# Kernel tuning notes

Measured on AMD Instinct MI355X. Metric: run time of the kernel, lower is better.

The kernel has to match this reference:

```python
import jax, jax.numpy as jnp
import numpy as np

NUM_HEADS = 16
D_MODEL = 1024
SEQ = 4096
HEAD_DIM = D_MODEL // NUM_HEADS
ROPE_BASE = 10000.0


def _rope(x):
    # x: [h, s, d]  (rotate-half RoPE per head)
    s, d = x.shape[-2], x.shape[-1]
    inv_freq = 1.0 / (ROPE_BASE ** (jnp.arange(0, d, 2, dtype=jnp.float32) / d))  # [d/2]
    ang = jnp.arange(s, dtype=jnp.float32)[:, None] * inv_freq[None, :]           # [s, d/2]
    cos, sin = jnp.cos(ang), jnp.sin(ang)
    x1, x2 = x[..., : d // 2], x[..., d // 2 :]
    return jnp.concatenate([x1 * cos - x2 * sin, x1 * sin + x2 * cos], axis=-1)


def setup_inputs() -> dict:
    key = jax.random.key(0)
    kq, kk, kv, kwq, kwk, kwv = jax.random.split(key, 6)
    scale = 1.0 / np.sqrt(D_MODEL)
    return {
        "q": jax.random.normal(kq, (SEQ, D_MODEL), dtype=jnp.float32),
        "k": jax.random.normal(kk, (SEQ, D_MODEL), dtype=jnp.float32),
        "v": jax.random.normal(kv, (SEQ, D_MODEL), dtype=jnp.float32),
        "mask": jnp.tril(jnp.ones((SEQ, SEQ), dtype=bool)),  # causal
        "Wq": jax.random.normal(kwq, (D_MODEL, D_MODEL), dtype=jnp.float32) * scale,
        "Wk": jax.random.normal(kwk, (D_MODEL, D_MODEL), dtype=jnp.float32) * scale,
        "Wv": jax.random.normal(kwv, (D_MODEL, D_MODEL), dtype=jnp.float32) * scale,
    }


def reference(q, k, v, mask, Wq, Wk, Wv):
    # Projections (eqx Linear: x @ W.T, no bias)
    qp = q @ Wq.T  # [s, d_model]
    kp = k @ Wk.T
    vp = v @ Wv.T
    # split heads: [s, (h d)] -> [h, s, d]
    def split(x):
        return x.reshape(SEQ, NUM_HEADS, HEAD_DIM).transpose(1, 0, 2)
    qh, kh, vh = split(qp), split(kp), split(vp)
    qh = _rope(qh)
    kh = _rope(kh)
    # explicit full logits, masked softmax (matches original, no SDPA)
    logits = jnp.einsum("hqd,hkd->hqk", qh, kh) / jnp.sqrt(jnp.float32(HEAD_DIM))
    logits = jnp.where(mask[None, :, :], logits, -jnp.inf)
    attn = jax.nn.softmax(logits, axis=-1)  # [h, q, k]
    out = jnp.einsum("hqk,hkd->hqd", attn, vh)
    return out.transpose(1, 0, 2).reshape(SEQ, D_MODEL)
```

## Files before the change

### kernel.cpp

```cpp
#include <hip/hip_runtime.h>
#include <math.h>

#define SEQ 4096
#define DMODEL 1024
#define NHEADS 16
#define HDIM 64

typedef __bf16 v8bf __attribute__((ext_vector_type(8)));
typedef float f32x4 __attribute__((ext_vector_type(4)));
typedef float f32x16 __attribute__((ext_vector_type(16)));
typedef int i32x2 __attribute__((ext_vector_type(2)));
typedef int i32x4 __attribute__((ext_vector_type(4)));

#define NPART 4608
#define SCALE_Q 0.18033688011112042f

__device__ __forceinline__ unsigned short f2bf(float f) {
    union { float f; unsigned int u; } v; v.f = f;
    unsigned int u = v.u;
    return (unsigned short)((u + 0x7fffu + ((u >> 16) & 1u)) >> 16);
}

__device__ __forceinline__ int cvtpk(float lo, float hi) {
    int r;
    asm("v_cvt_pk_bf16_f32 %0, %1, %2" : "=v"(r) : "v"(lo), "v"(hi));
    return r;
}

__device__ __forceinline__ void gload16(const unsigned short* g, unsigned short* l) {
    __builtin_amdgcn_global_load_lds(
        (const __attribute__((address_space(1))) unsigned int*)g,
        (__attribute__((address_space(3))) unsigned int*)l, 16, 0, 0);
}

__global__ __launch_bounds__(256) void cast_kernel(
    const float* __restrict__ q, const float* __restrict__ k, const float* __restrict__ v,
    const float* __restrict__ wq, const float* __restrict__ wk, const float* __restrict__ wv,
    unsigned short* __restrict__ xq, unsigned short* __restrict__ xk,
    unsigned short* __restrict__ xv, unsigned short* __restrict__ wb)
{
    const size_t M4 = (size_t)4 << 20, M1 = (size_t)1 << 20;
    size_t i = ((size_t)blockIdx.x * 256 + threadIdx.x) * 8;
    const float* s; unsigned short* d; size_t off;
    if (i < M4)                 { s = q;  d = xq;          off = i; }
    else if (i < 2 * M4)        { s = k;  d = xk;          off = i - M4; }
    else if (i < 3 * M4)        { s = v;  d = xv;          off = i - 2 * M4; }
    else if (i < 3 * M4 + M1)   { s = wq; d = wb;          off = i - 3 * M4; }
    else if (i < 3 * M4 + 2*M1) { s = wk; d = wb + M1;     off = i - 3 * M4 - M1; }
    else                        { s = wv; d = wb + 2 * M1; off = i - 3 * M4 - 2 * M1; }
    float4 a = *reinterpret_cast<const float4*>(s + off);
    float4 b = *reinterpret_cast<const float4*>(s + off + 4);
    uint4 u;
    u.x = (unsigned)cvtpk(a.x, a.y); u.y = (unsigned)cvtpk(a.z, a.w);
    u.z = (unsigned)cvtpk(b.x, b.y); u.w = (unsigned)cvtpk(b.z, b.w);
    *reinterpret_cast<uint4*>(d + off) = u;
}

__global__ __launch_bounds__(256) void rope_table_kernel(float2* __restrict__ tab)
{
    int idx = blockIdx.x * 256 + threadIdx.x;
    int m = idx >> 5;
    int j = idx & 31;
    float invf = expf(-(float)j * 0.28782313662425574f);
    float sn, cs;
    sincosf((float)m * invf, &sn, &cs);
    float2 t; t.x = cs; t.y = sn;
    tab[idx] = t;
}

__global__ __launch_bounds__(256) void proj_rope_kernel(
    const unsigned short* __restrict__ Xq, const unsigned short* __restrict__ Xk,
    const unsigned short* __restrict__ Xv, const unsigned short* __restrict__ Wb,
    const float2* __restrict__ rope_tab,
    unsigned short* __restrict__ qh, unsigned short* __restrict__ kfr,
    unsigned short* __restrict__ vfr)
{
    const int tz = blockIdx.z;
    const unsigned short* __restrict__ X = (tz == 0) ? Xq : (tz == 1) ? Xk : Xv;
    const unsigned short* __restrict__ W = Wb + (size_t)tz * ((size_t)1 << 20);

    const int tid = threadIdx.x;
    const int lane = tid & 63;
    const int wid = tid >> 6;
    const int l15 = lane & 15;
    const int l4 = lane >> 4;
    const int wr = wid >> 1, wc = wid & 1;

    const int m0 = blockIdx.x * 128;
    const int n0 = blockIdx.y * 128;

    __shared__ __align__(16) unsigned short Ab[2][4096];
    __shared__ __align__(16) unsigned short Bb[2][4096];

    int grow[2], gcol[2];
    #pragma unroll
    for (int g = 0; g < 2; ++g) {
        int row = wid * 32 + g * 16 + (lane >> 2);
        grow[g] = row;
        gcol[g] = 8 * ((lane & 3) ^ ((row >> 1) & 3));
    }

    auto STAGE = [&](int b, int kt) {
        const int k0 = kt << 5;
        #pragma unroll
        for (int g = 0; g < 2; ++g) {
            gload16(X + (size_t)(m0 + grow[g]) * DMODEL + k0 + gcol[g],
                    &Ab[b][(wid * 2 + g) * 512]);
            gload16(W + (size_t)(n0 + grow[g]) * DMODEL + k0 + gcol[g],
                    &Bb[b][(wid * 2 + g) * 512]);
        }
    };

    f32x4 acc[4][4] = {};

    STAGE(0, 0);
    for (int kt = 0; kt < 32; ++kt) {
        __syncthreads();
        if (kt < 31) STAGE((kt + 1) & 1, kt + 1);

        const unsigned short* A = Ab[kt & 1];
        const unsigned short* B = Bb[kt & 1];

        v8bf af[4], bfr[4];
        #pragma unroll
        for (int mi = 0; mi < 4; ++mi) {
            int row = wr * 64 + mi * 16 + l15;
            int byte = row * 64 + ((l4 ^ ((row >> 1) & 3)) << 4);
            af[mi] = *reinterpret_cast<const v8bf*>(reinterpret_cast<const char*>(A) + byte);
        }
        #pragma unroll
        for (int ni = 0; ni < 4; ++ni) {
            int row = wc * 64 + ni * 16 + l15;
            int byte = row * 64 + ((l4 ^ ((row >> 1) & 3)) << 4);
            bfr[ni] = *reinterpret_cast<const v8bf*>(reinterpret_cast<const char*>(B) + byte);
        }
        #pragma unroll
        for (int mi = 0; mi < 4; ++mi)
            #pragma unroll
            for (int ni = 0; ni < 4; ++ni)
                acc[mi][ni] = __builtin_amdgcn_mfma_f32_16x16x32_bf16(af[mi], bfr[ni], acc[mi][ni], 0, 0, 0);
    }

    const int h = (n0 >> 6) + wc;
    const int mbase = m0 + wr * 64;
    const int T = blockIdx.x * 2 + wr;

    if (tz == 2) {
        unsigned short* vb = vfr + (size_t)h * 262144 + (size_t)T * 4096;
        #pragma unroll
        for (int mi = 0; mi < 4; ++mi) {
            #pragma unroll
            for (int ni = 0; ni < 4; ++ni) {
                int f = (ni >> 1) * 4 + mi;
                int off = f * 512 + ((l4 >> 1) * 32 + (ni & 1) * 16 + l15) * 8 + (l4 & 1) * 4;
                uint2 pk;
                pk.x = (unsigned)cvtpk(acc[mi][ni][0], acc[mi][ni][1]);
                pk.y = (unsigned)cvtpk(acc[mi][ni][2], acc[mi][ni][3]);
                *reinterpret_cast<uint2*>(vb + off) = pk;
            }
        }
    } else if (tz == 1) {
        unsigned short* kb = kfr + (size_t)h * 262144 + (size_t)T * 4096;
        #pragma unroll
        for (int ni = 0; ni < 2; ++ni) {
            int j = ni * 16 + l15;
            #pragma unroll
            for (int mi = 0; mi < 4; ++mi) {
                #pragma unroll
                for (int r = 0; r < 4; ++r) {
                    int m = mbase + mi * 16 + l4 * 4 + r;
                    float2 t = rope_tab[m * 32 + j];
                    float cs = t.x, sn = t.y;
                    float x1 = acc[mi][ni][r];
                    float x2 = acc[mi][ni + 2][r];
                    int rowoff = ((l15 >> 3) * 32 + (mi & 1) * 16 + l4 * 4 + r) * 8 + (l15 & 7);
                    int fb = (mi >> 1) * 4;
                    kb[(fb + ni) * 512 + rowoff]     = f2bf(x1 * cs - x2 * sn);
                    kb[(fb + ni + 2) * 512 + rowoff] = f2bf(x1 * sn + x2 * cs);
                }
            }
        }
    } else {
        unsigned short* base = qh + (size_t)h * SEQ * HDIM;
        #pragma unroll
        for (int ni = 0; ni < 2; ++ni) {
            int j = ni * 16 + l15;
            #pragma unroll
            for (int mi = 0; mi < 4; ++mi) {
                #pragma unroll
                for (int r = 0; r < 4; ++r) {
                    int m = mbase + mi * 16 + l4 * 4 + r;
                    float2 t = rope_tab[m * 32 + j];
                    float cs = t.x * SCALE_Q, sn = t.y * SCALE_Q;
                    float x1 = acc[mi][ni][r];
                    float x2 = acc[mi][ni + 2][r];
                    base[(size_t)m * HDIM + j]      = f2bf(x1 * cs - x2 * sn);
                    base[(size_t)m * HDIM + j + 32] = f2bf(x1 * sn + x2 * cs);
                }
            }
        }
    }
}

__global__ __launch_bounds__(256, 2) void attn_kernel(
    const unsigned short* __restrict__ qh, const unsigned short* __restrict__ kfr,
    const unsigned short* __restrict__ vfr, float* __restrict__ out,
    unsigned short* __restrict__ po, float* __restrict__ ml)
{
    const int tid = threadIdx.x;
    const int lane = tid & 63;
    const int wid = tid >> 6;
    const int l31 = lane & 31;
    const int l5 = lane >> 5;

    const int bid = blockIdx.x;
    const int xcd = bid & 7;
    const int idx = bid >> 3;
    const int c4 = idx * 4 + wid;
    const int hsel = (c4 >= 320) ? 1 : 0;
    const int h = (xcd << 1) | hsel;
    const int r = 319 - (c4 - hsel * 320);

    int qb, c, nc;
    if (r < 32)       { qb = r;                     c = 0;            nc = 1; }
    else if (r < 96)  { qb = 32 + ((r - 32) >> 1);  c = (r - 32) & 1; nc = 2; }
    else if (r < 192) { int rr = r - 96; qb = 64 + rr / 3; c = rr - (qb - 64) * 3; nc = 3; }
    else              { int rr = r - 192; qb = 96 + (rr >> 2); c = rr & 3; nc = 4; }

    const int q0 = qb * 32;
    const int q = q0 + l31;
    const int nt = (q0 + 32 + 63) >> 6;
    const int t0 = c * 16;
    const int t1 = min(t0 + 16, nt);

    const unsigned short* __restrict__ qbase = qh + ((size_t)h * SEQ + q) * HDIM + l5 * 8;
    const unsigned short* __restrict__ kfh = kfr + (size_t)h * 262144 + lane * 8;
    const unsigned short* __restrict__ vfh = vfr + (size_t)h * 262144 + lane * 8;

    v8bf qf[4];
    #pragma unroll
    for (int dk = 0; dk < 4; ++dk)
        qf[dk] = *reinterpret_cast<const v8bf*>(qbase + dk * 16);

    f32x16 of[2] = {};
    float lreg = 0.0f;

    auto LOADK = [&](v8bf (&KB)[8], int T) {
        const unsigned short* kp = kfh + (size_t)T * 4096;
        #pragma unroll
        for (int f = 0; f < 8; ++f)
            KB[f] = *reinterpret_cast<const v8bf*>(kp + f * 512);
    };

    auto ROUND = [&](int T, v8bf (&KC)[8], v8bf (&KN)[8]) {
        v8bf vf[8];
        {
            const unsigned short* vp = vfh + (size_t)T * 4096;
            #pragma unroll
            for (int f = 0; f < 8; ++f)
                vf[f] = *reinterpret_cast<const v8bf*>(vp + f * 512);
        }
        if (T + 1 < t1) LOADK(KN, T + 1);

        f32x16 st[2];
        #pragma unroll
        for (int ns = 0; ns < 2; ++ns) {
            f32x16 acc = {};
            #pragma unroll
            for (int dk = 0; dk < 4; ++dk)
                acc = __builtin_amdgcn_mfma_f32_32x32x16_bf16(KC[ns * 4 + dk], qf[dk], acc, 0, 0, 0);
            st[ns] = acc;
        }

        if (T == nt - 1) {
            const int kvb = T * 64 + 4 * l5;
            #pragma unroll
            for (int ns = 0; ns < 2; ++ns)
                #pragma unroll
                for (int i = 0; i < 16; ++i) {
                    int kv = kvb + ns * 32 + (i & 3) + 8 * (i >> 2);
                    if (kv > q) st[ns][i] = -INFINITY;
                }
        }

        float ps0 = 0.f, ps1 = 0.f, ps2 = 0.f, ps3 = 0.f;
        #pragma unroll
        for (int ns = 0; ns < 2; ++ns)
            #pragma unroll
            for (int i = 0; i < 16; ++i) {
                float p = exp2f(st[ns][i]);
                st[ns][i] = p;
                if ((i & 3) == 0) ps0 += p; else if ((i & 3) == 1) ps1 += p;
                else if ((i & 3) == 2) ps2 += p; else ps3 += p;
            }
        lreg += (ps0 + ps1) + (ps2 + ps3);

        v8bf pt[4];
        #pragma unroll
        for (int kb = 0; kb < 4; ++kb) {
            int ns = kb >> 1, kp = (kb & 1) * 8;
            int A0 = cvtpk(st[ns][kp + 0], st[ns][kp + 1]);
            int A1 = cvtpk(st[ns][kp + 2], st[ns][kp + 3]);
            int B0 = cvtpk(st[ns][kp + 4], st[ns][kp + 5]);
            int B1 = cvtpk(st[ns][kp + 6], st[ns][kp + 7]);
            i32x2 s0 = __builtin_amdgcn_permlane32_swap(A0, B0, false, false);
            i32x2 s1 = __builtin_amdgcn_permlane32_swap(A1, B1, false, false);
            i32x4 u; u.x = s0.x; u.y = s1.x; u.z = s0.y; u.w = s1.y;
            v8bf p; __builtin_memcpy(&p, &u, 16);
            pt[kb] = p;
        }

        #pragma unroll
        for (int dt = 0; dt < 2; ++dt)
            #pragma unroll
            for (int kb = 0; kb < 4; ++kb)
                of[dt] = __builtin_amdgcn_mfma_f32_32x32x16_bf16(vf[dt * 4 + kb], pt[kb], of[dt], 0, 0, 0);
    };

    v8bf kA[8], kB[8];
    LOADK(kA, t0);
    int t = t0;
    while (true) {
        ROUND(t, kA, kB);
        if (++t == t1) break;
        ROUND(t, kB, kA);
        if (++t == t1) break;
    }

    {
        i32x2 sw = __builtin_amdgcn_permlane32_swap(__float_as_int(lreg), __float_as_int(lreg), false, false);
        lreg = __int_as_float(sw.x) + __int_as_float(sw.y);
    }

    if (nc == 1) {
        float inv = 1.0f / lreg;
        float* obase = out + (size_t)q * DMODEL + h * HDIM + l5 * 4;
        #pragma unroll
        for (int dt = 0; dt < 2; ++dt)
            #pragma unroll
            for (int g = 0; g < 4; ++g) {
                f32x4 o4;
                o4[0] = of[dt][g * 4 + 0] * inv;
                o4[1] = of[dt][g * 4 + 1] * inv;
                o4[2] = of[dt][g * 4 + 2] * inv;
                o4[3] = of[dt][g * 4 + 3] * inv;
                *reinterpret_cast<f32x4*>(obase + dt * 32 + g * 8) = o4;
            }
    } else {
        const int p = h * 288 + (r - 32);
        unsigned short* pb = po + ((size_t)p * 32 + l31) * 64 + l5 * 4;
        #pragma unroll
        for (int dt = 0; dt < 2; ++dt)
            #pragma unroll
            for (int g = 0; g < 4; ++g) {
                uint2 u;
                u.x = (unsigned)cvtpk(of[dt][g * 4 + 0], of[dt][g * 4 + 1]);
                u.y = (unsigned)cvtpk(of[dt][g * 4 + 2], of[dt][g * 4 + 3]);
                *reinterpret_cast<uint2*>(pb + dt * 32 + g * 8) = u;
            }
        if (l5 == 0) {
            float2 v; v.x = 0.0f; v.y = lreg;
            reinterpret_cast<float2*>(ml)[(size_t)p * 32 + l31] = v;
        }
    }
}

__global__ __launch_bounds__(256) void combine_kernel(
    const unsigned short* __restrict__ po, const float* __restrict__ ml,
    float* __restrict__ out)
{
    const int b = blockIdx.x;
    const int h = b / 96;
    const int j = b - h * 96;
    const int qb = 32 + j;
    int nc, r0;
    if (qb < 64)      { nc = 2; r0 = 32 + ((qb - 32) << 1); }
    else if (qb < 96) { nc = 3; r0 = 96 + (qb - 64) * 3; }
    else              { nc = 4; r0 = 192 + ((qb - 96) << 2); }
    const int p0 = h * 288 + (r0 - 32);
    const int d = threadIdx.x & 63;
    const int rg = threadIdx.x >> 6;
    const int q0 = qb * 32;

    for (int row = rg; row < 32; row += 4) {
        float L = 0.0f, O = 0.0f;
        #pragma unroll
        for (int ci = 0; ci < 4; ++ci)
            if (ci < nc) {
                float2 v = reinterpret_cast<const float2*>(ml)[(size_t)(p0 + ci) * 32 + row];
                L += v.y;
                unsigned int raw = po[((size_t)(p0 + ci) * 32 + row) * 64 + d];
                union { unsigned int u; float f; } cv; cv.u = raw << 16;
                O += cv.f;
            }
        out[(size_t)(q0 + row) * DMODEL + h * HDIM + d] = O / L;
    }
}

extern "C" void kernel_launch(void* const* d_in, const int* in_sizes, int n_in,
                              void* d_out, int out_size, void* d_ws, size_t ws_size,
                              hipStream_t stream) {
    (void)in_sizes; (void)n_in; (void)out_size; (void)ws_size;
    const float* q  = (const float*)d_in[0];
    const float* k  = (const float*)d_in[1];
    const float* v  = (const float*)d_in[2];
    const float* Wq = (const float*)d_in[4];
    const float* Wk = (const float*)d_in[5];
    const float* Wv = (const float*)d_in[6];

    const size_t M4 = (size_t)4 << 20;
    unsigned short* qh  = (unsigned short*)d_ws;
    unsigned short* kfr = qh  + M4;
    unsigned short* vfr = kfr + M4;
    unsigned short* scratch = vfr + M4;
    unsigned short* Xbv = scratch;
    unsigned short* Wb  = scratch + M4;
    float2* rope_tab = (float2*)(Wb + 3 * ((size_t)1 << 20));
    unsigned short* po  = scratch;
    float* ml = (float*)(po + (size_t)NPART * 32 * 64);
    unsigned short* Xbq = (unsigned short*)d_out;
    unsigned short* Xbk = Xbq + M4;
    float* out = (float*)d_out;

    cast_kernel<<<dim3(7680), 256, 0, stream>>>(q, k, v, Wq, Wk, Wv, Xbq, Xbk, Xbv, Wb);
    rope_table_kernel<<<dim3(512), 256, 0, stream>>>(rope_tab);

    dim3 g1(SEQ / 128, DMODEL / 128, 3);
    proj_rope_kernel<<<g1, 256, 0, stream>>>(Xbq, Xbk, Xbv, Wb, rope_tab, qh, kfr, vfr);

    attn_kernel<<<dim3(1280), 256, 0, stream>>>(qh, kfr, vfr, out, po, ml);

    combine_kernel<<<dim3(16 * 96), 256, 0, stream>>>(po, ml, out);
}
```

Before: 145.8 us.

## Share K/V tiles across four waves via LDS in attention; fuse rope table into cast

The attention kernel now gives each block a 128-row query tile, with each of the four waves handling 32 rows. K and V tiles are staged once per block into double-buffered shared memory using global_load_lds, instead of each wave loading them from global memory into registers. This cuts repeated global K/V traffic, at the cost of block-wide barriers per tile and idle waves on the diagonal tiles. The partial-result indexing and the combine kernel are remapped to the new work split, and the rope-table kernel is folded into extra blocks of the cast kernel to save a launch.

```diff
diff --git a/kernel.cpp b/kernel.cpp
--- a/kernel.cpp
+++ b/kernel.cpp
@@ -37,8 +37,20 @@
     const float* __restrict__ q, const float* __restrict__ k, const float* __restrict__ v,
     const float* __restrict__ wq, const float* __restrict__ wk, const float* __restrict__ wv,
     unsigned short* __restrict__ xq, unsigned short* __restrict__ xk,
-    unsigned short* __restrict__ xv, unsigned short* __restrict__ wb)
+    unsigned short* __restrict__ xv, unsigned short* __restrict__ wb,
+    float2* __restrict__ tab)
 {
+    if (blockIdx.x >= 7680) {
+        int idx = (blockIdx.x - 7680) * 256 + threadIdx.x;
+        int m = idx >> 5;
+        int j = idx & 31;
+        float invf = expf(-(float)j * 0.28782313662425574f);
+        float sn, cs;
+        sincosf((float)m * invf, &sn, &cs);
+        float2 t; t.x = cs; t.y = sn;
+        tab[idx] = t;
+        return;
+    }
     const size_t M4 = (size_t)4 << 20, M1 = (size_t)1 << 20;
     size_t i = ((size_t)blockIdx.x * 256 + threadIdx.x) * 8;
     const float* s; unsigned short* d; size_t off;
@@ -56,18 +68,6 @@
     *reinterpret_cast<uint4*>(d + off) = u;
 }
 
-__global__ __launch_bounds__(256) void rope_table_kernel(float2* __restrict__ tab)
-{
-    int idx = blockIdx.x * 256 + threadIdx.x;
-    int m = idx >> 5;
-    int j = idx & 31;
-    float invf = expf(-(float)j * 0.28782313662425574f);
-    float sn, cs;
-    sincosf((float)m * invf, &sn, &cs);
-    float2 t; t.x = cs; t.y = sn;
-    tab[idx] = t;
-}
-
 __global__ __launch_bounds__(256) void proj_rope_kernel(
     const unsigned short* __restrict__ Xq, const unsigned short* __restrict__ Xk,
     const unsigned short* __restrict__ Xv, const unsigned short* __restrict__ Wb,
@@ -216,115 +216,119 @@
     const int bid = blockIdx.x;
     const int xcd = bid & 7;
     const int idx = bid >> 3;
-    const int c4 = idx * 4 + wid;
-    const int hsel = (c4 >= 320) ? 1 : 0;
+    const int hsel = (idx >= 80) ? 1 : 0;
     const int h = (xcd << 1) | hsel;
-    const int r = 319 - (c4 - hsel * 320);
-
-    int qb, c, nc;
-    if (r < 32)       { qb = r;                     c = 0;            nc = 1; }
-    else if (r < 96)  { qb = 32 + ((r - 32) >> 1);  c = (r - 32) & 1; nc = 2; }
-    else if (r < 192) { int rr = r - 96; qb = 64 + rr / 3; c = rr - (qb - 64) * 3; nc = 3; }
-    else              { int rr = r - 192; qb = 96 + (rr >> 2); c = rr & 3; nc = 4; }
-
-    const int q0 = qb * 32;
-    const int q = q0 + l31;
-    const int nt = (q0 + 32 + 63) >> 6;
+    const int j = 79 - (idx - hsel * 80);
+
+    int qb, c, nc, mc = 0;
+    if (j < 8) { qb = j; c = 0; nc = 1; }
+    else {
+        mc = j - 8;
+        if (mc < 16)      { qb = 8  + (mc >> 1);         c = mc & 1;         nc = 2; }
+        else if (mc < 40) { qb = 16 + (mc - 16) / 3;     c = (mc - 16) % 3;  nc = 3; }
+        else              { qb = 24 + ((mc - 40) >> 2);  c = (mc - 40) & 3;  nc = 4; }
+    }
+
+    const int q0 = qb * 128;
+    const int qr0 = q0 + wid * 32;
+    const int q = qr0 + l31;
+    const int nt = 2 * qb + 2;
     const int t0 = c * 16;
     const int t1 = min(t0 + 16, nt);
-
-    const unsigned short* __restrict__ qbase = qh + ((size_t)h * SEQ + q) * HDIM + l5 * 8;
-    const unsigned short* __restrict__ kfh = kfr + (size_t)h * 262144 + lane * 8;
-    const unsigned short* __restrict__ vfh = vfr + (size_t)h * 262144 + lane * 8;
+    const int tmax = (qr0 + 31) >> 6;
+
+    __shared__ __align__(16) unsigned short Kb[2][4096];
+    __shared__ __align__(16) unsigned short Vb[2][4096];
+
+    const unsigned short* __restrict__ kfh = kfr + (size_t)h * 262144;
+    const unsigned short* __restrict__ vfh = vfr + (size_t)h * 262144;
 
     v8bf qf[4];
-    #pragma unroll
-    for (int dk = 0; dk < 4; ++dk)
-        qf[dk] = *reinterpret_cast<const v8bf*>(qbase + dk * 16);
+    {
+        const unsigned short* qbase = qh + ((size_t)h * SEQ + q) * HDIM + l5 * 8;
+        #pragma unroll
+        for (int dk = 0; dk < 4; ++dk)
+            qf[dk] = *reinterpret_cast<const v8bf*>(qbase + dk * 16);
+    }
+
+    auto STAGE = [&](int b, int T) {
+        const size_t toff = (size_t)T * 4096;
+        const unsigned short* ks = kfh + toff + wid * 512 + lane * 8;
+        const unsigned short* vs = vfh + toff + wid * 512 + lane * 8;
+        gload16(ks,        &Kb[b][wid * 512]);
+        gload16(ks + 2048, &Kb[b][wid * 512 + 2048]);
+        gload16(vs,        &Vb[b][wid * 512]);
+        gload16(vs + 2048, &Vb[b][wid * 512 + 2048]);
+    };
 
     f32x16 of[2] = {};
     float lreg = 0.0f;
 
-    auto LOADK = [&](v8bf (&KB)[8], int T) {
-        const unsigned short* kp = kfh + (size_t)T * 4096;
-        #pragma unroll
-        for (int f = 0; f < 8; ++f)
-            KB[f] = *reinterpret_cast<const v8bf*>(kp + f * 512);
-    };
-
-    auto ROUND = [&](int T, v8bf (&KC)[8], v8bf (&KN)[8]) {
-        v8bf vf[8];
-        {
-            const unsigned short* vp = vfh + (size_t)T * 4096;
-            #pragma unroll
-            for (int f = 0; f < 8; ++f)
-                vf[f] = *reinterpret_cast<const v8bf*>(vp + f * 512);
-        }
-        if (T + 1 < t1) LOADK(KN, T + 1);
-
-        f32x16 st[2];
-        #pragma unroll
-        for (int ns = 0; ns < 2; ++ns) {
-            f32x16 acc = {};
-            #pragma unroll
-            for (int dk = 0; dk < 4; ++dk)
-                acc = __builtin_amdgcn_mfma_f32_32x32x16_bf16(KC[ns * 4 + dk], qf[dk], acc, 0, 0, 0);
-            st[ns] = acc;
-        }
-
-        if (T == nt - 1) {
-            const int kvb = T * 64 + 4 * l5;
+    STAGE(0, t0);
+    for (int t = t0; t < t1; ++t) {
+        __syncthreads();
+        const int b = (t - t0) & 1;
+        if (t + 1 < t1) STAGE(b ^ 1, t + 1);
+
+        if (t <= tmax) {
+            f32x16 st[2];
+            #pragma unroll
+            for (int ns = 0; ns < 2; ++ns) {
+                f32x16 acc = {};
+                #pragma unroll
+                for (int dk = 0; dk < 4; ++dk) {
+                    v8bf kf = *reinterpret_cast<const v8bf*>(&Kb[b][(ns * 4 + dk) * 512 + lane * 8]);
+                    acc = __builtin_amdgcn_mfma_f32_32x32x16_bf16(kf, qf[dk], acc, 0, 0, 0);
+                }
+                st[ns] = acc;
+            }
+
+            if (t == tmax) {
+                const int kvb = t * 64 + 4 * l5;
+                #pragma unroll
+                for (int ns = 0; ns < 2; ++ns)
+                    #pragma unroll
+                    for (int i = 0; i < 16; ++i) {
+                        int kv = kvb + ns * 32 + (i & 3) + 8 * (i >> 2);
+                        if (kv > q) st[ns][i] = -INFINITY;
+                    }
+            }
+
+            float ps0 = 0.f, ps1 = 0.f, ps2 = 0.f, ps3 = 0.f;
             #pragma unroll
             for (int ns = 0; ns < 2; ++ns)
                 #pragma unroll
                 for (int i = 0; i < 16; ++i) {
-                    int kv = kvb + ns * 32 + (i & 3) + 8 * (i >> 2);
-                    if (kv > q) st[ns][i] = -INFINITY;
+                    float p = exp2f(st[ns][i]);
+                    st[ns][i] = p;
+                    if ((i & 3) == 0) ps0 += p; else if ((i & 3) == 1) ps1 += p;
+                    else if ((i & 3) == 2) ps2 += p; else ps3 += p;
                 }
-        }
-
-        float ps0 = 0.f, ps1 = 0.f, ps2 = 0.f, ps3 = 0.f;
-        #pragma unroll
-        for (int ns = 0; ns < 2; ++ns)
-            #pragma unroll
-            for (int i = 0; i < 16; ++i) {
-                float p = exp2f(st[ns][i]);
-                st[ns][i] = p;
-                if ((i & 3) == 0) ps0 += p; else if ((i & 3) == 1) ps1 += p;
-                else if ((i & 3) == 2) ps2 += p; else ps3 += p;
-            }
-        lreg += (ps0 + ps1) + (ps2 + ps3);
-
-        v8bf pt[4];
-        #pragma unroll
-        for (int kb = 0; kb < 4; ++kb) {
-            int ns = kb >> 1, kp = (kb & 1) * 8;
-            int A0 = cvtpk(st[ns][kp + 0], st[ns][kp + 1]);
-            int A1 = cvtpk(st[ns][kp + 2], st[ns][kp + 3]);
-            int B0 = cvtpk(st[ns][kp + 4], st[ns][kp + 5]);
-            int B1 = cvtpk(st[ns][kp + 6], st[ns][kp + 7]);
-            i32x2 s0 = __builtin_amdgcn_permlane32_swap(A0, B0, false, false);
-            i32x2 s1 = __builtin_amdgcn_permlane32_swap(A1, B1, false, false);
-            i32x4 u; u.x = s0.x; u.y = s1.x; u.z = s0.y; u.w = s1.y;
-            v8bf p; __builtin_memcpy(&p, &u, 16);
-            pt[kb] = p;
-        }
-
-        #pragma unroll
-        for (int dt = 0; dt < 2; ++dt)
-            #pragma unroll
-            for (int kb = 0; kb < 4; ++kb)
-                of[dt] = __builtin_amdgcn_mfma_f32_32x32x16_bf16(vf[dt * 4 + kb], pt[kb], of[dt], 0, 0, 0);
-    };
-
-    v8bf kA[8], kB[8];
-    LOADK(kA, t0);
-    int t = t0;
-    while (true) {
-        ROUND(t, kA, kB);
-        if (++t == t1) break;
-        ROUND(t, kB, kA);
-        if (++t == t1) break;
+            lreg += (ps0 + ps1) + (ps2 + ps3);
+
+            v8bf pt[4];
+            #pragma unroll
+            for (int kb = 0; kb < 4; ++kb) {
+                int ns = kb >> 1, kp = (kb & 1) * 8;
+                int A0 = cvtpk(st[ns][kp + 0], st[ns][kp + 1]);
+                int A1 = cvtpk(st[ns][kp + 2], st[ns][kp + 3]);
+                int B0 = cvtpk(st[ns][kp + 4], st[ns][kp + 5]);
+                int B1 = cvtpk(st[ns][kp + 6], st[ns][kp + 7]);
+                i32x2 s0 = __builtin_amdgcn_permlane32_swap(A0, B0, false, false);
+                i32x2 s1 = __builtin_amdgcn_permlane32_swap(A1, B1, false, false);
+                i32x4 u; u.x = s0.x; u.y = s1.x; u.z = s0.y; u.w = s1.y;
+                v8bf p; __builtin_memcpy(&p, &u, 16);
+                pt[kb] = p;
+            }
+
+            #pragma unroll
+            for (int dt = 0; dt < 2; ++dt)
+                #pragma unroll
+                for (int kb = 0; kb < 4; ++kb) {
+                    v8bf vf = *reinterpret_cast<const v8bf*>(&Vb[b][(dt * 4 + kb) * 512 + lane * 8]);
+                    of[dt] = __builtin_amdgcn_mfma_f32_32x32x16_bf16(vf, pt[kb], of[dt], 0, 0, 0);
+                }
+        }
     }
 
     {
@@ -347,7 +351,7 @@
                 *reinterpret_cast<f32x4*>(obase + dt * 32 + g * 8) = o4;
             }
     } else {
-        const int p = h * 288 + (r - 32);
+        const int p = h * 288 + mc * 4 + wid;
         unsigned short* pb = po + ((size_t)p * 32 + l31) * 64 + l5 * 4;
         #pragma unroll
         for (int dt = 0; dt < 2; ++dt)
@@ -371,25 +375,27 @@
 {
     const int b = blockIdx.x;
     const int h = b / 96;
-    const int j = b - h * 96;
-    const int qb = 32 + j;
-    int nc, r0;
-    if (qb < 64)      { nc = 2; r0 = 32 + ((qb - 32) << 1); }
-    else if (qb < 96) { nc = 3; r0 = 96 + (qb - 64) * 3; }
-    else              { nc = 4; r0 = 192 + ((qb - 96) << 2); }
-    const int p0 = h * 288 + (r0 - 32);
+    const int rem = b - h * 96;
+    const int qb = 8 + (rem >> 2);
+    const int w = rem & 3;
+    int nc, mcs;
+    if (qb < 16)      { nc = 2; mcs = (qb - 8) * 2; }
+    else if (qb < 24) { nc = 3; mcs = 16 + (qb - 16) * 3; }
+    else              { nc = 4; mcs = 40 + (qb - 24) * 4; }
+    const int pbase = h * 288 + mcs * 4 + w;
     const int d = threadIdx.x & 63;
     const int rg = threadIdx.x >> 6;
-    const int q0 = qb * 32;
+    const int q0 = qb * 128 + w * 32;
 
     for (int row = rg; row < 32; row += 4) {
         float L = 0.0f, O = 0.0f;
         #pragma unroll
         for (int ci = 0; ci < 4; ++ci)
             if (ci < nc) {
-                float2 v = reinterpret_cast<const float2*>(ml)[(size_t)(p0 + ci) * 32 + row];
+                int p = pbase + ci * 4;
+                float2 v = reinterpret_cast<const float2*>(ml)[(size_t)p * 32 + row];
                 L += v.y;
-                unsigned int raw = po[((size_t)(p0 + ci) * 32 + row) * 64 + d];
+                unsigned int raw = po[((size_t)p * 32 + row) * 64 + d];
                 union { unsigned int u; float f; } cv; cv.u = raw << 16;
                 O += cv.f;
             }
@@ -422,8 +428,7 @@
     unsigned short* Xbk = Xbq + M4;
     float* out = (float*)d_out;
 
-    cast_kernel<<<dim3(7680), 256, 0, stream>>>(q, k, v, Wq, Wk, Wv, Xbq, Xbk, Xbv, Wb);
-    rope_table_kernel<<<dim3(512), 256, 0, stream>>>(rope_tab);
+    cast_kernel<<<dim3(8192), 256, 0, stream>>>(q, k, v, Wq, Wk, Wv, Xbq, Xbk, Xbv, Wb, rope_tab);
 
     dim3 g1(SEQ / 128, DMODEL / 128, 3);
     proj_rope_kernel<<<g1, 256, 0, stream>>>(Xbq, Xbk, Xbv, Wb, rope_tab, qh, kfr, vfr);
```

After: 147.3 us. About the same (+1.0%).
